# Optimization experiments

Hardware: AMD Instinct MI355X
Metric: run time of the kernel (lower is better)

## Reference

```python
import jax, jax.numpy as jnp
import numpy as np

B, T, D, H = 4, 1024, 512, 8
DH = D // H
L = 2 * T - 1  # relative positions


def setup_inputs() -> dict:
    key = jax.random.key(0)
    ks = jax.random.split(key, 16)
    s = 0.02
    return {
        "x": jax.random.normal(ks[0], (B, T, D), jnp.float32),
        "pos_emb": jax.random.normal(ks[1], (L, D), jnp.float32),
        "Wq": jax.random.normal(ks[2], (D, D), jnp.float32) * s,
        "bq": jnp.zeros((D,), jnp.float32),
        "Wk": jax.random.normal(ks[3], (D, D), jnp.float32) * s,
        "bk": jnp.zeros((D,), jnp.float32),
        "Wv": jax.random.normal(ks[4], (D, D), jnp.float32) * s,
        "bv": jnp.zeros((D,), jnp.float32),
        "Wr": jax.random.normal(ks[5], (D, D), jnp.float32) * s,
        "Wo": jax.random.normal(ks[6], (D, D), jnp.float32) * s,
        "bo": jnp.zeros((D,), jnp.float32),
        "u": jax.random.normal(ks[7], (H, DH), jnp.float32) * s,
        "v": jax.random.normal(ks[8], (H, DH), jnp.float32) * s,
        "ln_gamma": jnp.ones((D,), jnp.float32),
        "ln_beta": jnp.zeros((D,), jnp.float32),
    }


def _rel_shift(x):
    # x: [B,H,T,2T-1] -> [B,H,T,T] (Transformer-XL/Conformer relative shift)
    b, h, q, l = x.shape
    x = jnp.pad(x, ((0, 0), (0, 0), (0, 0), (1, 0)))
    x = x.reshape(b, h, l + 1, q)
    x = x[:, :, 1:, :].reshape(b, h, q, l)
    return x[..., :q]


def reference(x, pos_emb, Wq, bq, Wk, bk, Wv, bv, Wr, Wo, bo, u, v, ln_gamma, ln_beta):
    # Faithful to source: layernorm output is computed but DISCARDED
    mu = jnp.mean(x, axis=-1, keepdims=True)
    var = jnp.mean((x - mu) ** 2, axis=-1, keepdims=True)
    _ln = (x - mu) * jax.lax.rsqrt(var + 1e-5) * ln_gamma + ln_beta  # unused (dead code in source)

    q = (x @ Wq + bq).reshape(B, T, H, DH)
    k = (x @ Wk + bk).reshape(B, T, H, DH)
    val = (x @ Wv + bv).reshape(B, T, H, DH)
    r = (pos_emb @ Wr).reshape(L, H, DH)

    # content term (AC) and position term (BD), Transformer-XL style
    ac = jnp.einsum("bqhd,bkhd->bhqk", q + u, k)
    bd = jnp.einsum("bqhd,lhd->bhql", q + v, r)
    bd = _rel_shift(bd)

    scores = (ac + bd) / np.sqrt(DH).astype(np.float32)
    attn = jax.nn.softmax(scores, axis=-1)  # dropout is identity in eval
    out = jnp.einsum("bhqk,bkhd->bqhd", attn, val).reshape(B, T, D)
    return out @ Wo + bo
```

## Files before the change

kernel.cpp:

```cpp
#include <hip/hip_runtime.h>

#define B_ 4
#define T_ 1024
#define D_ 512
#define H_ 8
#define DH_ 64
#define L_ 2047

typedef __attribute__((ext_vector_type(8))) short bf16x8;
typedef __attribute__((ext_vector_type(4))) float f32x4;
typedef __attribute__((ext_vector_type(8))) unsigned short us8v;
typedef __attribute__((ext_vector_type(4))) unsigned short us4v;

__device__ __forceinline__ void split_bf16(float a, unsigned short& h, unsigned short& l) {
  unsigned u = __float_as_uint(a);
  h = (unsigned short)(u >> 16);
  float hf = __uint_as_float(u & 0xFFFF0000u);
  l = (unsigned short)(__float_as_uint(a - hf) >> 16);
}
__device__ __forceinline__ float bf2f(unsigned short s) {
  return __uint_as_float(((unsigned)s) << 16);
}
__device__ __forceinline__ void gload16(const unsigned short* g, unsigned short* l) {
  __builtin_amdgcn_global_load_lds(
      (const __attribute__((address_space(1))) void*)g,
      (__attribute__((address_space(3))) void*)l, 16, 0, 0);
}

__global__ __launch_bounds__(256)
void conv_flat(const float* __restrict__ x, unsigned short* __restrict__ xh,
               unsigned short* __restrict__ xl,
               const float* __restrict__ p, unsigned short* __restrict__ ph,
               unsigned short* __restrict__ pl) {
  int blk = blockIdx.x;
  const float* in; unsigned short* oh; unsigned short* ol; long n, base;
  if (blk < 2048) { in = x; oh = xh; ol = xl; n = 2097152; base = (long)blk * 1024; }
  else { in = p; oh = ph; ol = pl; n = 1048064; base = (long)(blk - 2048) * 1024; }
  long i = base + threadIdx.x * 4;
  if (i + 4 <= n) {
    float4 a = *(const float4*)&in[i];
    us4v h, l; unsigned short th, tl;
    split_bf16(a.x, th, tl); h[0] = th; l[0] = tl;
    split_bf16(a.y, th, tl); h[1] = th; l[1] = tl;
    split_bf16(a.z, th, tl); h[2] = th; l[2] = tl;
    split_bf16(a.w, th, tl); h[3] = th; l[3] = tl;
    *(us4v*)&oh[i] = h; *(us4v*)&ol[i] = l;
  } else {
    for (long e = i; e < n; ++e) {
      unsigned short th, tl; split_bf16(in[e], th, tl); oh[e] = th; ol[e] = tl;
    }
  }
}

__global__ __launch_bounds__(256)
void conv_wt(const float* w0, const float* w1, const float* w2, const float* w3,
             const float* w4, unsigned short* __restrict__ wth,
             unsigned short* __restrict__ wtl) {
  const float* W = blockIdx.z == 0 ? w0 : blockIdx.z == 1 ? w1 :
                   blockIdx.z == 2 ? w2 : blockIdx.z == 3 ? w3 : w4;
  unsigned short* oh = wth + (long)blockIdx.z * 262144;
  unsigned short* ol = wtl + (long)blockIdx.z * 262144;
  __shared__ unsigned short Th[64][72], Tl[64][72];
  const int k0 = blockIdx.x * 64, n0 = blockIdx.y * 64;
  const int tid = threadIdx.x;
#pragma unroll
  for (int m = 0; m < 4; ++m) {
    int s = tid + 256 * m;
    int kk = s >> 4, n4 = (s & 15) * 4;
    float4 a = *(const float4*)&W[(long)(k0 + kk) * 512 + n0 + n4];
    unsigned short th, tl;
    split_bf16(a.x, th, tl); Th[n4 + 0][kk] = th; Tl[n4 + 0][kk] = tl;
    split_bf16(a.y, th, tl); Th[n4 + 1][kk] = th; Tl[n4 + 1][kk] = tl;
    split_bf16(a.z, th, tl); Th[n4 + 2][kk] = th; Tl[n4 + 2][kk] = tl;
    split_bf16(a.w, th, tl); Th[n4 + 3][kk] = th; Tl[n4 + 3][kk] = tl;
  }
  __syncthreads();
#pragma unroll
  for (int m = 0; m < 2; ++m) {
    int s = tid + 256 * m;
    int nn = s >> 3, kb = (s & 7) * 8;
    *(us8v*)&oh[(long)(n0 + nn) * 512 + k0 + kb] = *(const us8v*)&Th[nn][kb];
    *(us8v*)&ol[(long)(n0 + nn) * 512 + k0 + kb] = *(const us8v*)&Tl[nn][kb];
  }
}

struct EpCfg {
  const unsigned short* wth;
  const unsigned short* wtl;
  const float* bias;
  float* cf;
  unsigned short* ch;
  unsigned short* cl;
  int ep;
};

__global__ __launch_bounds__(256)
void gemm4(const unsigned short* __restrict__ Ag_h, const unsigned short* __restrict__ Ag_l,
           EpCfg e0, EpCfg e1, EpCfg e2, int mlimit) {
  __shared__ unsigned short SMEM[24576];

  const int tid = threadIdx.x;
  const int row0 = blockIdx.x * 128;
  const int cg0 = blockIdx.y * 64;
  const int wsel = cg0 >> 9;
  const int col0 = cg0 & 511;
  const EpCfg C = wsel == 0 ? e0 : (wsel == 1 ? e1 : e2);

  const int lane = tid & 63;
  const int w = tid >> 6;
  const int wr = (w >> 1) * 64;
  const int wc = (w & 1) * 32;
  const int frow = lane & 15;
  const int lg = lane >> 4;
  const int mlim1 = mlimit - 1;

  const int lrow = lane >> 2;
  const int lcs = (((lane & 3) ^ ((lane >> 3) & 3)) << 3);

#define STAGE(base, kt) do {                                                   \
    const int k0s = (kt) * 32;                                                 \
    _Pragma("unroll")                                                          \
    for (int cc = 0; cc < 2; ++cc) {                                           \
      int c = w + 4 * cc;                                                      \
      int gr = min(row0 + (c << 4) + lrow, mlim1);                             \
      long gi = (long)gr * 512 + k0s + lcs;                                    \
      gload16(&Ag_h[gi], &SMEM[(base) + (c << 9)]);                            \
      gload16(&Ag_l[gi], &SMEM[(base) + 4096 + (c << 9)]);                     \
    }                                                                          \
    { int gc = col0 + (w << 4) + lrow;                                         \
      long gi = (long)gc * 512 + k0s + lcs;                                    \
      gload16(&C.wth[gi], &SMEM[(base) + 8192 + (w << 9)]);                    \
      gload16(&C.wtl[gi], &SMEM[(base) + 10240 + (w << 9)]); }                 \
  } while (0)

  f32x4 acc[4][2];
#pragma unroll
  for (int a = 0; a < 4; ++a)
#pragma unroll
    for (int bb = 0; bb < 2; ++bb) acc[a][bb] = (f32x4){0.f, 0.f, 0.f, 0.f};

  STAGE(0, 0);
  __syncthreads();

  for (int t = 0; t < 16; ++t) {
    const int cur = (t & 1) * 12288;
    if (t < 15) STAGE(12288 - cur, t + 1);

    const unsigned short* Abh = &SMEM[cur];
    const unsigned short* Abl = &SMEM[cur + 4096];
    const unsigned short* Bbh = &SMEM[cur + 8192];
    const unsigned short* Bbl = &SMEM[cur + 10240];

    bf16x8 bhf[2], blf[2];
#pragma unroll
    for (int bb = 0; bb < 2; ++bb) {
      int rB = wc + bb * 16 + frow;
      int off = rB * 32 + ((lg ^ ((rB >> 1) & 3)) << 3);
      bhf[bb] = *(const bf16x8*)&Bbh[off];
      blf[bb] = *(const bf16x8*)&Bbl[off];
    }
#pragma unroll
    for (int a = 0; a < 4; ++a) {
      int rA = wr + a * 16 + frow;
      int offA = rA * 32 + ((lg ^ ((rA >> 1) & 3)) << 3);
      bf16x8 ah = *(const bf16x8*)&Abh[offA];
      bf16x8 al = *(const bf16x8*)&Abl[offA];
#pragma unroll
      for (int bb = 0; bb < 2; ++bb) {
        acc[a][bb] = __builtin_amdgcn_mfma_f32_16x16x32_bf16(ah, bhf[bb], acc[a][bb], 0, 0, 0);
        acc[a][bb] = __builtin_amdgcn_mfma_f32_16x16x32_bf16(ah, blf[bb], acc[a][bb], 0, 0, 0);
        acc[a][bb] = __builtin_amdgcn_mfma_f32_16x16x32_bf16(al, bhf[bb], acc[a][bb], 0, 0, 0);
      }
    }
    __syncthreads();
  }
#undef STAGE

  const int lg4 = (lane >> 4) * 4;

  if (C.ep == 0) {
#pragma unroll
    for (int bb = 0; bb < 2; ++bb) {
      int col = col0 + wc + bb * 16 + frow;
      float bv = C.bias ? C.bias[col] : 0.f;
#pragma unroll
      for (int a = 0; a < 4; ++a) {
#pragma unroll
        for (int g = 0; g < 4; ++g) {
          int row = row0 + wr + a * 16 + lg4 + g;
          if (row < mlimit) C.cf[(long)row * 512 + col] = acc[a][bb][g] + bv;
        }
      }
    }
  } else if (C.ep == 1) {
    unsigned short (*Th)[72] = (unsigned short (*)[72])&SMEM[0];
    unsigned short (*Tl)[72] = (unsigned short (*)[72])&SMEM[4608];
#pragma unroll
    for (int p = 0; p < 2; ++p) {
      __syncthreads();
      if ((wr >> 6) == p) {
#pragma unroll
        for (int bb = 0; bb < 2; ++bb) {
          int clx = wc + bb * 16 + frow;
          float bv = C.bias ? C.bias[col0 + clx] : 0.f;
#pragma unroll
          for (int a = 0; a < 4; ++a) {
#pragma unroll
            for (int g = 0; g < 4; ++g) {
              unsigned short th, tl;
              split_bf16(acc[a][bb][g] + bv, th, tl);
              int rlx = a * 16 + lg4 + g;
              Th[rlx][clx] = th; Tl[rlx][clx] = tl;
            }
          }
        }
      }
      __syncthreads();
#pragma unroll
      for (int m = 0; m < 2; ++m) {
        int s = tid + 256 * m;
        int rr = s >> 3, cb = (s & 7) * 8;
        int row = row0 + p * 64 + rr;
        if (row < mlimit) {
          long gi = (long)row * 512 + col0 + cb;
          *(us8v*)&C.ch[gi] = *(const us8v*)&Th[rr][cb];
          *(us8v*)&C.cl[gi] = *(const us8v*)&Tl[rr][cb];
        }
      }
    }
  } else {
    unsigned short (*Th)[136] = (unsigned short (*)[136])&SMEM[0];
    unsigned short (*Tl)[136] = (unsigned short (*)[136])&SMEM[8704];
    int bbat = row0 >> 10, tok0 = row0 & 1023;
#pragma unroll
    for (int bb = 0; bb < 2; ++bb) {
      int clx = wc + bb * 16 + frow;
      float bv = C.bias ? C.bias[col0 + clx] : 0.f;
#pragma unroll
      for (int a = 0; a < 4; ++a) {
#pragma unroll
        for (int g = 0; g < 4; ++g) {
          int rlx = wr + a * 16 + lg4 + g;
          unsigned short th, tl;
          split_bf16(acc[a][bb][g] + bv, th, tl);
          Th[clx][rlx] = th; Tl[clx][rlx] = tl;
        }
      }
    }
    __syncthreads();
#pragma unroll
    for (int m = 0; m < 4; ++m) {
      int s = tid + 256 * m;
      int dd = s >> 4, tb = (s & 15) * 8;
      int colg = col0 + dd;
      long gi = (((long)bbat * 8 + (colg >> 6)) * 64 + (colg & 63)) * 1024 + tok0 + tb;
      *(us8v*)&C.ch[gi] = *(const us8v*)&Th[dd][tb];
      *(us8v*)&C.cl[gi] = *(const us8v*)&Tl[dd][tb];
    }
  }
}

__global__ __launch_bounds__(256)
void ukvr_kernel(const unsigned short* __restrict__ kh, const unsigned short* __restrict__ kl,
                 const unsigned short* __restrict__ rh, const unsigned short* __restrict__ rl,
                 const float* __restrict__ u, const float* __restrict__ v,
                 float* __restrict__ uk, float* __restrict__ vr) {
  int wg = (blockIdx.x * 256 + threadIdx.x) >> 6;
  int lane = threadIdx.x & 63;
  int hh = lane >> 3;
  int d8 = (lane & 7) * 8;
  bool isuk = wg < 4096;
  const unsigned short* sh; const unsigned short* sl; const float* cf; long row;
  if (isuk) { sh = kh; sl = kl; cf = u; row = wg; }
  else { sh = rh; sl = rl; cf = v; row = min(wg - 4096, L_ - 1); }
  long gi = row * 512 + hh * 64 + d8;
  us8v ah = *(const us8v*)&sh[gi];
  us8v al = *(const us8v*)&sl[gi];
  float part = 0.f;
#pragma unroll
  for (int e = 0; e < 8; ++e)
    part += cf[hh * 64 + d8 + e] * (bf2f(ah[e]) + bf2f(al[e]));
  part += __shfl_xor(part, 1);
  part += __shfl_xor(part, 2);
  part += __shfl_xor(part, 4);
  if ((lane & 7) == 0) {
    if (isuk) uk[(wg >> 10) * 8192 + hh * 1024 + (wg & 1023)] = part;
    else vr[hh * 2048 + (wg - 4096)] = part;
  }
}

__global__ __launch_bounds__(512)
void attn_mfma2(const unsigned short* __restrict__ qhp, const unsigned short* __restrict__ qlp,
                const unsigned short* __restrict__ kh, const unsigned short* __restrict__ kl,
                const unsigned short* __restrict__ vth, const unsigned short* __restrict__ vtl,
                const unsigned short* __restrict__ rh, const unsigned short* __restrict__ rl,
                const float* __restrict__ uk, const float* __restrict__ vr,
                unsigned short* __restrict__ oh, unsigned short* __restrict__ ol) {
  const int qt = blockIdx.x, h = blockIdx.y, b = blockIdx.z;
  const int q0 = qt * 128;
  const int tid = threadIdx.x;
  const int lane = tid & 63;
  const int wid = tid >> 6;
  const int lr = lane & 15;
  const int lg = lane >> 4;

  __shared__ unsigned short Kh[64][68], Kl[64][68];
  __shared__ unsigned short Vh[64][68], Vl[64][68];
  __shared__ unsigned short RWh[192][68], RWl[192][68];
  __shared__ unsigned short Ph[128][68], Pl[128][68];

  bf16x8 quh[2], qul[2];
  {
    long qoff = (long)(b * T_ + q0 + wid * 16 + lr) * 512 + h * 64 + lg * 8;
    quh[0] = *(const bf16x8*)&qhp[qoff];
    quh[1] = *(const bf16x8*)&qhp[qoff + 32];
    qul[0] = *(const bf16x8*)&qlp[qoff];
    qul[1] = *(const bf16x8*)&qlp[qoff + 32];
  }

  f32x4 pv[4];
#pragma unroll
  for (int c = 0; c < 4; ++c) pv[c] = (f32x4){0.f, 0.f, 0.f, 0.f};
  float m_run[4], l_run[4];
#pragma unroll
  for (int r = 0; r < 4; ++r) { m_run[r] = -3.0e38f; l_run[r] = 0.f; }

  const int band0 = 112 - wid * 16;
  const int sbase0 = 14 - 2 * qt;
  const float* ukrow = uk + ((long)b * 8 + h) * 1024;
  const float* vrrow = vr + (long)h * 2048;
  const int stj = tid >> 3;
  const int std8 = (tid & 7) * 8;

  for (int t = 0; t < 16; ++t) {
    const int j0 = t * 64;
    __syncthreads();

    { long gi = (long)(b * T_ + j0 + stj) * 512 + h * 64 + std8;
      *(us8v*)&Kh[stj][std8] = *(const us8v*)&kh[gi];
      *(us8v*)&Kl[stj][std8] = *(const us8v*)&kl[gi]; }
    { long gi = (((long)b * 8 + h) * 64 + stj) * 1024 + j0 + std8;
      *(us8v*)&Vh[stj][std8] = *(const us8v*)&vth[gi];
      *(us8v*)&Vl[stj][std8] = *(const us8v*)&vtl[gi]; }
    if (t == 0) {
#pragma unroll
      for (int ss = 0; ss < 2; ++ss) {
        int seg = sbase0 + ss;
        int slot = seg % 3;
        long A = min(seg * 64 + stj, L_ - 1);
        long gi = A * 512 + h * 64 + std8;
        *(us8v*)&RWh[slot * 64 + stj][std8] = *(const us8v*)&rh[gi];
        *(us8v*)&RWl[slot * 64 + stj][std8] = *(const us8v*)&rl[gi];
      }
    }
    { int seg = sbase0 + t + 2;
      int slot = seg % 3;
      long A = min(seg * 64 + stj, L_ - 1);
      long gi = A * 512 + h * 64 + std8;
      *(us8v*)&RWh[slot * 64 + stj][std8] = *(const us8v*)&rh[gi];
      *(us8v*)&RWl[slot * 64 + stj][std8] = *(const us8v*)&rl[gi]; }
    __syncthreads();

    f32x4 ac[4], bda[5];
#pragma unroll
    for (int c = 0; c < 4; ++c) ac[c] = (f32x4){0.f, 0.f, 0.f, 0.f};
#pragma unroll
    for (int c = 0; c < 5; ++c) bda[c] = (f32x4){0.f, 0.f, 0.f, 0.f};

#pragma unroll
    for (int ks = 0; ks < 2; ++ks) {
#pragma unroll
      for (int c = 0; c < 4; ++c) {
        bf16x8 kbh = *(const bf16x8*)&Kh[c * 16 + lr][ks * 32 + lg * 8];
        bf16x8 kbl = *(const bf16x8*)&Kl[c * 16 + lr][ks * 32 + lg * 8];
        ac[c] = __builtin_amdgcn_mfma_f32_16x16x32_bf16(quh[ks], kbh, ac[c], 0, 0, 0);
        ac[c] = __builtin_amdgcn_mfma_f32_16x16x32_bf16(quh[ks], kbl, ac[c], 0, 0, 0);
        ac[c] = __builtin_amdgcn_mfma_f32_16x16x32_bf16(qul[ks], kbh, ac[c], 0, 0, 0);
      }
#pragma unroll
      for (int c = 0; c < 5; ++c) {
        int off = band0 + c * 16;
        int slot = (sbase0 + t + (off >> 6)) % 3;
        int rrow = slot * 64 + (off & 63) + lr;
        bf16x8 rbh = *(const bf16x8*)&RWh[rrow][ks * 32 + lg * 8];
        bf16x8 rbl = *(const bf16x8*)&RWl[rrow][ks * 32 + lg * 8];
        bda[c] = __builtin_amdgcn_mfma_f32_16x16x32_bf16(quh[ks], rbh, bda[c], 0, 0, 0);
        bda[c] = __builtin_amdgcn_mfma_f32_16x16x32_bf16(quh[ks], rbl, bda[c], 0, 0, 0);
        bda[c] = __builtin_amdgcn_mfma_f32_16x16x32_bf16(qul[ks], rbh, bda[c], 0, 0, 0);
      }
    }

    const int wbase = 896 - q0 + j0;
#pragma unroll
    for (int c = 0; c < 5; ++c) {
      float vv = vrrow[wbase + band0 + c * 16 + lr];
#pragma unroll
      for (int r = 0; r < 4; ++r) bda[c][r] += vv;
    }

    float p_[4][4];
#pragma unroll
    for (int r = 0; r < 4; ++r) {
      int rowl = lg * 4 + r;
      int e = lr - rowl + 15;
      int srcl = lg * 16 + (e & 15);
      int carry = e >> 4;
      float s0 = __shfl(bda[0][r], srcl);
      float s1 = __shfl(bda[1][r], srcl);
      float s2 = __shfl(bda[2][r], srcl);
      float s3 = __shfl(bda[3][r], srcl);
      float s4 = __shfl(bda[4][r], srcl);
      p_[0][r] = carry ? s1 : s0;
      p_[1][r] = carry ? s2 : s1;
      p_[2][r] = carry ? s3 : s2;
      p_[3][r] = carry ? s4 : s3;
    }
#pragma unroll
    for (int c = 0; c < 4; ++c) {
      float ukv = ukrow[j0 + c * 16 + lr];
#pragma unroll
      for (int r = 0; r < 4; ++r)
        p_[c][r] = (ac[c][r] + p_[c][r] + ukv) * 0.125f;
    }

#pragma unroll
    for (int r = 0; r < 4; ++r) {
      float lm = fmaxf(fmaxf(p_[0][r], p_[1][r]), fmaxf(p_[2][r], p_[3][r]));
#pragma unroll
      for (int off = 1; off < 16; off <<= 1)
        lm = fmaxf(lm, __shfl_xor(lm, off));
      float mnew = fmaxf(m_run[r], lm);
      float rescale = __expf(m_run[r] - mnew);
      float srow = 0.f;
#pragma unroll
      for (int c = 0; c < 4; ++c) {
        float pe = __expf(p_[c][r] - mnew);
        p_[c][r] = pe;
        srow += pe;
      }
#pragma unroll
      for (int off = 1; off < 16; off <<= 1)
        srow += __shfl_xor(srow, off);
      l_run[r] = l_run[r] * rescale + srow;
      m_run[r] = mnew;
#pragma unroll
      for (int c = 0; c < 4; ++c) pv[c][r] *= rescale;
    }

#pragma unroll
    for (int c = 0; c < 4; ++c)
#pragma unroll
      for (int r = 0; r < 4; ++r) {
        unsigned short th, tl;
        split_bf16(p_[c][r], th, tl);
        Ph[wid * 16 + lg * 4 + r][c * 16 + lr] = th;
        Pl[wid * 16 + lg * 4 + r][c * 16 + lr] = tl;
      }

#pragma unroll
    for (int ks = 0; ks < 2; ++ks) {
      bf16x8 pah = *(const bf16x8*)&Ph[wid * 16 + lr][ks * 32 + lg * 8];
      bf16x8 pal = *(const bf16x8*)&Pl[wid * 16 + lr][ks * 32 + lg * 8];
#pragma unroll
      for (int c = 0; c < 4; ++c) {
        bf16x8 vbh = *(const bf16x8*)&Vh[c * 16 + lr][ks * 32 + lg * 8];
        bf16x8 vbl = *(const bf16x8*)&Vl[c * 16 + lr][ks * 32 + lg * 8];
        pv[c] = __builtin_amdgcn_mfma_f32_16x16x32_bf16(pah, vbh, pv[c], 0, 0, 0);
        pv[c] = __builtin_amdgcn_mfma_f32_16x16x32_bf16(pah, vbl, pv[c], 0, 0, 0);
        pv[c] = __builtin_amdgcn_mfma_f32_16x16x32_bf16(pal, vbh, pv[c], 0, 0, 0);
      }
    }
  }

#pragma unroll
  for (int r = 0; r < 4; ++r) {
    float inv = 1.f / l_run[r];
    long base = (long)(b * T_ + q0 + wid * 16 + lg * 4 + r) * 512 + h * 64;
#pragma unroll
    for (int c = 0; c < 4; ++c) {
      unsigned short th, tl;
      split_bf16(pv[c][r] * inv, th, tl);
      oh[base + c * 16 + lr] = th;
      ol[base + c * 16 + lr] = tl;
    }
  }
}

extern "C" void kernel_launch(void* const* d_in, const int* in_sizes, int n_in,
                              void* d_out, int out_size, void* d_ws, size_t ws_size,
                              hipStream_t stream) {
  const float* x       = (const float*)d_in[0];
  const float* pos_emb = (const float*)d_in[1];
  const float* Wq      = (const float*)d_in[2];
  const float* bq      = (const float*)d_in[3];
  const float* Wk      = (const float*)d_in[4];
  const float* bk      = (const float*)d_in[5];
  const float* Wv      = (const float*)d_in[6];
  const float* bv      = (const float*)d_in[7];
  const float* Wr      = (const float*)d_in[8];
  const float* Wo      = (const float*)d_in[9];
  const float* bo      = (const float*)d_in[10];
  const float* u       = (const float*)d_in[11];
  const float* v       = (const float*)d_in[12];

  float* out = (float*)d_out;
  unsigned short* us = (unsigned short*)d_ws;
  const long S = 2097152;

  unsigned short* qh  = us;
  unsigned short* ql  = us + S;
  unsigned short* kh  = us + 2 * S;
  unsigned short* kl  = us + 3 * S;
  unsigned short* vth = us + 4 * S;
  unsigned short* vtl = us + 5 * S;
  unsigned short* rh  = us + 6 * S;
  unsigned short* rl  = rh + 1048576;
  unsigned short* xh  = us + 7 * S;
  unsigned short* xl  = us + 8 * S;
  unsigned short* ph  = us + 9 * S;
  unsigned short* pl  = ph + 1048576;
  unsigned short* wth = us + 10 * S;
  unsigned short* wtl = wth + 1310720;
  float* uk = (float*)(wtl + 1310720);
  float* vr = uk + 32768;

  conv_flat<<<3072, 256, 0, stream>>>(x, xh, xl, pos_emb, ph, pl);
  conv_wt<<<dim3(8, 8, 5), 256, 0, stream>>>(Wq, Wk, Wv, Wr, Wo, wth, wtl);

  EpCfg cq{wth,            wtl,            bq,      nullptr, qh,  ql,  1};
  EpCfg ck{wth + 262144,   wtl + 262144,   bk,      nullptr, kh,  kl,  1};
  EpCfg cv{wth + 524288,   wtl + 524288,   bv,      nullptr, vth, vtl, 2};
  gemm4<<<dim3(32, 24), 256, 0, stream>>>(xh, xl, cq, ck, cv, 4096);

  EpCfg cr{wth + 786432,   wtl + 786432,   nullptr, nullptr, rh,  rl,  1};
  gemm4<<<dim3(16, 8), 256, 0, stream>>>(ph, pl, cr, cr, cr, 2047);

  ukvr_kernel<<<1536, 256, 0, stream>>>(kh, kl, rh, rl, u, v, uk, vr);

  attn_mfma2<<<dim3(8, 8, 4), 512, 0, stream>>>(qh, ql, kh, kl, vth, vtl, rh, rl,
                                                uk, vr, xh, xl);

  EpCfg co{wth + 1048576,  wtl + 1048576,  bo,      out,     nullptr, nullptr, 0};
  gemm4<<<dim3(32, 8), 256, 0, stream>>>(xh, xl, co, co, co, 4096);
}
```

Baseline: 231.6 us.

## Prefetch next K/V/R tiles into registers and raise wave priority around MFMAs

```diff
diff --git a/kernel.cpp b/kernel.cpp
--- a/kernel.cpp
+++ b/kernel.cpp
@@ -332,34 +332,42 @@
   const int stj = tid >> 3;
   const int std8 = (tid & 7) * 8;
 
+  { long gi = (long)(b * T_ + stj) * 512 + h * 64 + std8;
+    *(us8v*)&Kh[stj][std8] = *(const us8v*)&kh[gi];
+    *(us8v*)&Kl[stj][std8] = *(const us8v*)&kl[gi]; }
+  { long gi = (((long)b * 8 + h) * 64 + stj) * 1024 + std8;
+    *(us8v*)&Vh[stj][std8] = *(const us8v*)&vth[gi];
+    *(us8v*)&Vl[stj][std8] = *(const us8v*)&vtl[gi]; }
+#pragma unroll
+  for (int ss = 0; ss < 3; ++ss) {
+    int seg = sbase0 + ss;
+    int slot = seg % 3;
+    long A = min(seg * 64 + stj, L_ - 1);
+    long gi = A * 512 + h * 64 + std8;
+    *(us8v*)&RWh[slot * 64 + stj][std8] = *(const us8v*)&rh[gi];
+    *(us8v*)&RWl[slot * 64 + stj][std8] = *(const us8v*)&rl[gi];
+  }
+  __syncthreads();
+
+  us8v rKh, rKl, rVh, rVl, rRh, rRl;
+#define LOADKV(tt) do {                                                        \
+    long giK = (long)(b * T_ + (tt) * 64 + stj) * 512 + h * 64 + std8;         \
+    rKh = *(const us8v*)&kh[giK];                                              \
+    rKl = *(const us8v*)&kl[giK];                                              \
+    long giV = (((long)b * 8 + h) * 64 + stj) * 1024 + (tt) * 64 + std8;       \
+    rVh = *(const us8v*)&vth[giV];                                             \
+    rVl = *(const us8v*)&vtl[giV];                                             \
+    int seg_ = sbase0 + (tt) + 2;                                              \
+    long A_ = min(seg_ * 64 + stj, L_ - 1);                                    \
+    long giR = A_ * 512 + h * 64 + std8;                                       \
+    rRh = *(const us8v*)&rh[giR];                                              \
+    rRl = *(const us8v*)&rl[giR];                                              \
+  } while (0)
+
+  LOADKV(1);
+
   for (int t = 0; t < 16; ++t) {
     const int j0 = t * 64;
-    __syncthreads();
-
-    { long gi = (long)(b * T_ + j0 + stj) * 512 + h * 64 + std8;
-      *(us8v*)&Kh[stj][std8] = *(const us8v*)&kh[gi];
-      *(us8v*)&Kl[stj][std8] = *(const us8v*)&kl[gi]; }
-    { long gi = (((long)b * 8 + h) * 64 + stj) * 1024 + j0 + std8;
-      *(us8v*)&Vh[stj][std8] = *(const us8v*)&vth[gi];
-      *(us8v*)&Vl[stj][std8] = *(const us8v*)&vtl[gi]; }
-    if (t == 0) {
-#pragma unroll
-      for (int ss = 0; ss < 2; ++ss) {
-        int seg = sbase0 + ss;
-        int slot = seg % 3;
-        long A = min(seg * 64 + stj, L_ - 1);
-        long gi = A * 512 + h * 64 + std8;
-        *(us8v*)&RWh[slot * 64 + stj][std8] = *(const us8v*)&rh[gi];
-        *(us8v*)&RWl[slot * 64 + stj][std8] = *(const us8v*)&rl[gi];
-      }
-    }
-    { int seg = sbase0 + t + 2;
-      int slot = seg % 3;
-      long A = min(seg * 64 + stj, L_ - 1);
-      long gi = A * 512 + h * 64 + std8;
-      *(us8v*)&RWh[slot * 64 + stj][std8] = *(const us8v*)&rh[gi];
-      *(us8v*)&RWl[slot * 64 + stj][std8] = *(const us8v*)&rl[gi]; }
-    __syncthreads();
 
     f32x4 ac[4], bda[5];
 #pragma unroll
@@ -367,6 +375,7 @@
 #pragma unroll
     for (int c = 0; c < 5; ++c) bda[c] = (f32x4){0.f, 0.f, 0.f, 0.f};
 
+    __builtin_amdgcn_s_setprio(1);
 #pragma unroll
     for (int ks = 0; ks < 2; ++ks) {
 #pragma unroll
@@ -389,6 +398,7 @@
         bda[c] = __builtin_amdgcn_mfma_f32_16x16x32_bf16(qul[ks], rbh, bda[c], 0, 0, 0);
       }
     }
+    __builtin_amdgcn_s_setprio(0);
 
     const int wbase = 896 - q0 + j0;
 #pragma unroll
@@ -457,6 +467,7 @@
         Pl[wid * 16 + lg * 4 + r][c * 16 + lr] = tl;
       }
 
+    __builtin_amdgcn_s_setprio(1);
 #pragma unroll
     for (int ks = 0; ks < 2; ++ks) {
       bf16x8 pah = *(const bf16x8*)&Ph[wid * 16 + lr][ks * 32 + lg * 8];
@@ -470,7 +481,23 @@
         pv[c] = __builtin_amdgcn_mfma_f32_16x16x32_bf16(pal, vbh, pv[c], 0, 0, 0);
       }
     }
-  }
+    __builtin_amdgcn_s_setprio(0);
+
+    if (t < 15) {
+      __syncthreads();
+      *(us8v*)&Kh[stj][std8] = rKh;
+      *(us8v*)&Kl[stj][std8] = rKl;
+      *(us8v*)&Vh[stj][std8] = rVh;
+      *(us8v*)&Vl[stj][std8] = rVl;
+      { int seg = sbase0 + t + 3;
+        int slot = seg % 3;
+        *(us8v*)&RWh[slot * 64 + stj][std8] = rRh;
+        *(us8v*)&RWl[slot * 64 + stj][std8] = rRl; }
+      if (t < 14) LOADKV(t + 2);
+      __syncthreads();
+    }
+  }
+#undef LOADKV
 
 #pragma unroll
   for (int r = 0; r < 4; ++r) {
```

Result: no change. 229.3 us (-1.0%).

## Split attention key range across two wave groups and merge softmax partials

Applied to the files above, without the earlier changes.

```diff
diff --git a/kernel.cpp b/kernel.cpp
--- a/kernel.cpp
+++ b/kernel.cpp
@@ -289,8 +289,8 @@
   }
 }
 
-__global__ __launch_bounds__(512)
-void attn_mfma2(const unsigned short* __restrict__ qhp, const unsigned short* __restrict__ qlp,
+__global__ __launch_bounds__(1024, 4)
+void attn_mfma3(const unsigned short* __restrict__ qhp, const unsigned short* __restrict__ qlp,
                 const unsigned short* __restrict__ kh, const unsigned short* __restrict__ kl,
                 const unsigned short* __restrict__ vth, const unsigned short* __restrict__ vtl,
                 const unsigned short* __restrict__ rh, const unsigned short* __restrict__ rl,
@@ -301,17 +301,23 @@
   const int tid = threadIdx.x;
   const int lane = tid & 63;
   const int wid = tid >> 6;
+  const int split = wid >> 3;
+  const int qwid = wid & 7;
   const int lr = lane & 15;
   const int lg = lane >> 4;
 
-  __shared__ unsigned short Kh[64][68], Kl[64][68];
-  __shared__ unsigned short Vh[64][68], Vl[64][68];
-  __shared__ unsigned short RWh[192][68], RWl[192][68];
-  __shared__ unsigned short Ph[128][68], Pl[128][68];
+  __shared__ union {
+    struct {
+      unsigned short Kh[2][64][68], Kl[2][64][68];
+      unsigned short Vh[2][64][68], Vl[2][64][68];
+    } s;
+    float scr[12288];
+  } U;
+  __shared__ unsigned short Ph[256][68], Pl[256][68];
 
   bf16x8 quh[2], qul[2];
   {
-    long qoff = (long)(b * T_ + q0 + wid * 16 + lr) * 512 + h * 64 + lg * 8;
+    long qoff = (long)(b * T_ + q0 + qwid * 16 + lr) * 512 + h * 64 + lg * 8;
     quh[0] = *(const bf16x8*)&qhp[qoff];
     quh[1] = *(const bf16x8*)&qhp[qoff + 32];
     qul[0] = *(const bf16x8*)&qlp[qoff];
@@ -325,40 +331,25 @@
 #pragma unroll
   for (int r = 0; r < 4; ++r) { m_run[r] = -3.0e38f; l_run[r] = 0.f; }
 
-  const int band0 = 112 - wid * 16;
-  const int sbase0 = 14 - 2 * qt;
+  const int band0 = 112 - qwid * 16;
   const float* ukrow = uk + ((long)b * 8 + h) * 1024;
   const float* vrrow = vr + (long)h * 2048;
-  const int stj = tid >> 3;
-  const int std8 = (tid & 7) * 8;
-
-  for (int t = 0; t < 16; ++t) {
+  const int stid = tid & 511;
+  const int stj = stid >> 3;
+  const int std8 = (stid & 7) * 8;
+  const long rcol = (long)h * 64;
+
+  for (int i = 0; i < 8; ++i) {
+    const int t = split * 8 + i;
     const int j0 = t * 64;
     __syncthreads();
 
     { long gi = (long)(b * T_ + j0 + stj) * 512 + h * 64 + std8;
-      *(us8v*)&Kh[stj][std8] = *(const us8v*)&kh[gi];
-      *(us8v*)&Kl[stj][std8] = *(const us8v*)&kl[gi]; }
+      *(us8v*)&U.s.Kh[split][stj][std8] = *(const us8v*)&kh[gi];
+      *(us8v*)&U.s.Kl[split][stj][std8] = *(const us8v*)&kl[gi]; }
     { long gi = (((long)b * 8 + h) * 64 + stj) * 1024 + j0 + std8;
-      *(us8v*)&Vh[stj][std8] = *(const us8v*)&vth[gi];
-      *(us8v*)&Vl[stj][std8] = *(const us8v*)&vtl[gi]; }
-    if (t == 0) {
-#pragma unroll
-      for (int ss = 0; ss < 2; ++ss) {
-        int seg = sbase0 + ss;
-        int slot = seg % 3;
-        long A = min(seg * 64 + stj, L_ - 1);
-        long gi = A * 512 + h * 64 + std8;
-        *(us8v*)&RWh[slot * 64 + stj][std8] = *(const us8v*)&rh[gi];
-        *(us8v*)&RWl[slot * 64 + stj][std8] = *(const us8v*)&rl[gi];
-      }
-    }
-    { int seg = sbase0 + t + 2;
-      int slot = seg % 3;
-      long A = min(seg * 64 + stj, L_ - 1);
-      long gi = A * 512 + h * 64 + std8;
-      *(us8v*)&RWh[slot * 64 + stj][std8] = *(const us8v*)&rh[gi];
-      *(us8v*)&RWl[slot * 64 + stj][std8] = *(const us8v*)&rl[gi]; }
+      *(us8v*)&U.s.Vh[split][stj][std8] = *(const us8v*)&vth[gi];
+      *(us8v*)&U.s.Vl[split][stj][std8] = *(const us8v*)&vtl[gi]; }
     __syncthreads();
 
     f32x4 ac[4], bda[5];
@@ -367,33 +358,35 @@
 #pragma unroll
     for (int c = 0; c < 5; ++c) bda[c] = (f32x4){0.f, 0.f, 0.f, 0.f};
 
+    const int wb = j0 - q0 + 896 + band0;
+
+    __builtin_amdgcn_s_setprio(1);
 #pragma unroll
     for (int ks = 0; ks < 2; ++ks) {
 #pragma unroll
       for (int c = 0; c < 4; ++c) {
-        bf16x8 kbh = *(const bf16x8*)&Kh[c * 16 + lr][ks * 32 + lg * 8];
-        bf16x8 kbl = *(const bf16x8*)&Kl[c * 16 + lr][ks * 32 + lg * 8];
+        bf16x8 kbh = *(const bf16x8*)&U.s.Kh[split][c * 16 + lr][ks * 32 + lg * 8];
+        bf16x8 kbl = *(const bf16x8*)&U.s.Kl[split][c * 16 + lr][ks * 32 + lg * 8];
         ac[c] = __builtin_amdgcn_mfma_f32_16x16x32_bf16(quh[ks], kbh, ac[c], 0, 0, 0);
         ac[c] = __builtin_amdgcn_mfma_f32_16x16x32_bf16(quh[ks], kbl, ac[c], 0, 0, 0);
         ac[c] = __builtin_amdgcn_mfma_f32_16x16x32_bf16(qul[ks], kbh, ac[c], 0, 0, 0);
       }
 #pragma unroll
       for (int c = 0; c < 5; ++c) {
-        int off = band0 + c * 16;
-        int slot = (sbase0 + t + (off >> 6)) % 3;
-        int rrow = slot * 64 + (off & 63) + lr;
-        bf16x8 rbh = *(const bf16x8*)&RWh[rrow][ks * 32 + lg * 8];
-        bf16x8 rbl = *(const bf16x8*)&RWl[rrow][ks * 32 + lg * 8];
+        int A = min(wb + c * 16 + lr, L_ - 1);
+        long off = (long)A * 512 + rcol + ks * 32 + lg * 8;
+        bf16x8 rbh = *(const bf16x8*)&rh[off];
+        bf16x8 rbl = *(const bf16x8*)&rl[off];
         bda[c] = __builtin_amdgcn_mfma_f32_16x16x32_bf16(quh[ks], rbh, bda[c], 0, 0, 0);
         bda[c] = __builtin_amdgcn_mfma_f32_16x16x32_bf16(quh[ks], rbl, bda[c], 0, 0, 0);
         bda[c] = __builtin_amdgcn_mfma_f32_16x16x32_bf16(qul[ks], rbh, bda[c], 0, 0, 0);
       }
     }
-
-    const int wbase = 896 - q0 + j0;
+    __builtin_amdgcn_s_setprio(0);
+
 #pragma unroll
     for (int c = 0; c < 5; ++c) {
-      float vv = vrrow[wbase + band0 + c * 16 + lr];
+      float vv = vrrow[wb + c * 16 + lr];
 #pragma unroll
       for (int r = 0; r < 4; ++r) bda[c][r] += vv;
     }
@@ -457,31 +450,55 @@
         Pl[wid * 16 + lg * 4 + r][c * 16 + lr] = tl;
       }
 
+    __builtin_amdgcn_s_setprio(1);
 #pragma unroll
     for (int ks = 0; ks < 2; ++ks) {
       bf16x8 pah = *(const bf16x8*)&Ph[wid * 16 + lr][ks * 32 + lg * 8];
       bf16x8 pal = *(const bf16x8*)&Pl[wid * 16 + lr][ks * 32 + lg * 8];
 #pragma unroll
       for (int c = 0; c < 4; ++c) {
-        bf16x8 vbh = *(const bf16x8*)&Vh[c * 16 + lr][ks * 32 + lg * 8];
-        bf16x8 vbl = *(const bf16x8*)&Vl[c * 16 + lr][ks * 32 + lg * 8];
+        bf16x8 vbh = *(const bf16x8*)&U.s.Vh[split][c * 16 + lr][ks * 32 + lg * 8];
+        bf16x8 vbl = *(const bf16x8*)&U.s.Vl[split][c * 16 + lr][ks * 32 + lg * 8];
         pv[c] = __builtin_amdgcn_mfma_f32_16x16x32_bf16(pah, vbh, pv[c], 0, 0, 0);
         pv[c] = __builtin_amdgcn_mfma_f32_16x16x32_bf16(pah, vbl, pv[c], 0, 0, 0);
         pv[c] = __builtin_amdgcn_mfma_f32_16x16x32_bf16(pal, vbh, pv[c], 0, 0, 0);
       }
     }
-  }
-
-#pragma unroll
-  for (int r = 0; r < 4; ++r) {
-    float inv = 1.f / l_run[r];
-    long base = (long)(b * T_ + q0 + wid * 16 + lg * 4 + r) * 512 + h * 64;
-#pragma unroll
-    for (int c = 0; c < 4; ++c) {
-      unsigned short th, tl;
-      split_bf16(pv[c][r] * inv, th, tl);
-      oh[base + c * 16 + lr] = th;
-      ol[base + c * 16 + lr] = tl;
+    __builtin_amdgcn_s_setprio(0);
+  }
+
+  __syncthreads();
+  const int slot = ((qwid * 64) + lane) * 24;
+  if (split == 1) {
+#pragma unroll
+    for (int c = 0; c < 4; ++c)
+#pragma unroll
+      for (int r = 0; r < 4; ++r) U.scr[slot + c * 4 + r] = pv[c][r];
+#pragma unroll
+    for (int r = 0; r < 4; ++r) {
+      U.scr[slot + 16 + r] = m_run[r];
+      U.scr[slot + 20 + r] = l_run[r];
+    }
+  }
+  __syncthreads();
+  if (split == 0) {
+#pragma unroll
+    for (int r = 0; r < 4; ++r) {
+      float m2 = U.scr[slot + 16 + r];
+      float l2 = U.scr[slot + 20 + r];
+      float m = fmaxf(m_run[r], m2);
+      float a1 = __expf(m_run[r] - m);
+      float a2 = __expf(m2 - m);
+      float inv = 1.f / (l_run[r] * a1 + l2 * a2);
+      long base = (long)(b * T_ + q0 + qwid * 16 + lg * 4 + r) * 512 + h * 64;
+#pragma unroll
+      for (int c = 0; c < 4; ++c) {
+        float val = (pv[c][r] * a1 + U.scr[slot + c * 4 + r] * a2) * inv;
+        unsigned short th, tl;
+        split_bf16(val, th, tl);
+        oh[base + c * 16 + lr] = th;
+        ol[base + c * 16 + lr] = tl;
+      }
     }
   }
 }
@@ -537,8 +554,8 @@
 
   ukvr_kernel<<<1536, 256, 0, stream>>>(kh, kl, rh, rl, u, v, uk, vr);
 
-  attn_mfma2<<<dim3(8, 8, 4), 512, 0, stream>>>(qh, ql, kh, kl, vth, vtl, rh, rl,
-                                                uk, vr, xh, xl);
+  attn_mfma3<<<dim3(8, 8, 4), 1024, 0, stream>>>(qh, ql, kh, kl, vth, vtl, rh, rl,
+                                                 uk, vr, xh, xl);
 
   EpCfg co{wth + 1048576,  wtl + 1048576,  bo,      out,     nullptr, nullptr, 0};
   gemm4<<<dim3(32, 8), 256, 0, stream>>>(xh, xl, co, co, co, 4096);
```

Measured after the change: 290.3 us. 25.4% more time.
